# Performance work log

Measured on AMD Instinct MI355X. Metric: run time of the kernel, lower is better.

The kernel has to match this reference:

```python
import math
import jax, jax.numpy as jnp
import numpy as np

S = 2  # scale_factor
IN_CH = 256
OFFSET_FACTOR = math.sqrt(128.0 / IN_CH)


def setup_inputs() -> dict:
    key = jax.random.key(0)
    k1, k2, k3 = jax.random.split(key, 3)
    x = jax.random.normal(k1, (4, IN_CH, 128, 128), jnp.float32)
    conv_w = jax.random.normal(k2, (2 * S * S, IN_CH, 1, 1), jnp.float32) * 0.01
    conv_b = jax.random.normal(k3, (2 * S * S,), jnp.float32) * 0.01
    return {"x": x, "conv_w": conv_w, "conv_b": conv_b}


def reference(x, conv_w, conv_b):
    b, c, H, W = x.shape
    s = S
    # 1x1 conv producing per-subpixel (x, y) offsets: [b, 2*s*s, H, W]
    out = jnp.einsum('bchw,oc->bohw', x, conv_w[:, :, 0, 0]) + conv_b[None, :, None, None]
    o1, o2 = jnp.split(out, 2, axis=1)  # each [b, s*s, H, W]
    # sub-pixel bias grid (meshgrid 'xy'): X[i,j]=x[j], Y[i,j]=y[i]
    sub = jnp.arange(0.0, 1.0, 1.0 / s)
    xb, yb = jnp.meshgrid(sub, sub, indexing='xy')  # [s, s]
    xb = xb.reshape(1, -1, 1, 1)
    yb = yb.reshape(1, -1, 1, 1)
    o1 = OFFSET_FACTOR * o1 + jnp.arange(W)[None, None, None, :] + xb  # x coords (pixels)
    o2 = OFFSET_FACTOR * o2 + jnp.arange(H)[None, None, :, None] + yb  # y coords (pixels)
    # [b,2,s,s,H,W] -> [b,2,H,s,W,s] -> [b,2,N], N = s*H*s*W
    off = jnp.stack((o1, o2), axis=1).reshape(b, 2, s, s, H, W)
    off = off.transpose(0, 1, 4, 2, 5, 3).reshape(b, 2, -1)
    xc, yc = off[:, 0], off[:, 1]  # [b, N]
    x0 = jnp.floor(xc)
    y0 = jnp.floor(yc)
    fx = xc - x0
    fy = yc - y0
    x0i = jnp.clip(x0.astype(jnp.int32), 0, W - 1)
    x1i = jnp.clip(x0.astype(jnp.int32) + 1, 0, W - 1)
    y0i = jnp.clip(y0.astype(jnp.int32), 0, H - 1)
    y1i = jnp.clip(y0.astype(jnp.int32) + 1, 0, H - 1)
    bidx = jnp.arange(b)[:, None]

    def gather(yi, xi):
        return x[bidx, :, yi, xi]  # [b, N, c]

    val = (gather(y0i, x0i) * ((1 - fx) * (1 - fy))[..., None]
           + gather(y0i, x1i) * (fx * (1 - fy))[..., None]
           + gather(y1i, x0i) * ((1 - fx) * fy)[..., None]
           + gather(y1i, x1i) * (fx * fy)[..., None])  # [b, N, c]
    return val.transpose(0, 2, 1).reshape(b, c, s * H, s * W)
```

## Files before the change

### kernel.cpp

```cpp
#include <hip/hip_runtime.h>
#include <math.h>

#define BATCH 4
#define C 256
#define H 128
#define W 128
#define HW (H * W)
#define OH 256
#define OW 256
#define NPIX (BATCH * HW)
#define NPOS (BATCH * OH * OW)
#define KSPLIT 4
#define KCH (C / KSPLIT)
#define CCHUNKS 4
__device__ __constant__ float OFF_FACTOR = 0.70710678118654752f;

__global__ __launch_bounds__(256) void conv_desc_kernel(
    const float* __restrict__ x, const float* __restrict__ cw,
    const float* __restrict__ cb, float2* __restrict__ desc) {
    __shared__ float sw[8 * C];
    __shared__ __align__(16) float red[KSPLIT * 8 * 256];
    int t = threadIdx.x;

    #pragma unroll
    for (int i = 0; i < 8; ++i) sw[i * 256 + t] = cw[i * 256 + t];
    __syncthreads();

    int k = t >> 6;
    int q = t & 63;
    int g4 = blockIdx.x * 64 + q;
    int g = g4 * 4;
    int b = g >> 14;
    int pix = g & (HW - 1);
    const float* xp = x + (size_t)b * C * HW + (size_t)(k * KCH) * HW + pix;

    float4 acc[8];
    #pragma unroll
    for (int o = 0; o < 8; ++o) acc[o] = make_float4(0.f, 0.f, 0.f, 0.f);

    #pragma unroll 8
    for (int c = 0; c < KCH; ++c) {
        float4 v = *(const float4*)(xp + (size_t)c * HW);
        #pragma unroll
        for (int o = 0; o < 8; ++o) {
            float wv = sw[o * C + k * KCH + c];
            acc[o].x += v.x * wv; acc[o].y += v.y * wv;
            acc[o].z += v.z * wv; acc[o].w += v.w * wv;
        }
    }

    #pragma unroll
    for (int o = 0; o < 8; ++o)
        *(float4*)&red[((k * 8 + o) << 8) + (q << 2)] = acc[o];
    __syncthreads();

    int g2 = blockIdx.x * 256 + t;
    int b2 = g2 >> 14;
    int pix2 = g2 & (HW - 1);
    int h2 = pix2 >> 7;
    int w2 = pix2 & (W - 1);

    float s[8];
    #pragma unroll
    for (int o = 0; o < 8; ++o) {
        float a = cb[o];
        #pragma unroll
        for (int kk = 0; kk < KSPLIT; ++kk)
            a += red[((kk * 8 + o) << 8) + t];
        s[o] = a;
    }

    #pragma unroll
    for (int sy = 0; sy < 2; ++sy) {
        int j0 = sy * 2;
        float yb = (float)h2 + 0.5f * (float)sy;
        float xc0 = OFF_FACTOR * s[j0]     + (float)w2;
        float yc0 = OFF_FACTOR * s[4 + j0] + yb;
        float xc1 = OFF_FACTOR * s[j0 + 1] + (float)w2 + 0.5f;
        float yc1 = OFF_FACTOR * s[5 + j0] + yb;
        int p = (b2 * OH + 2 * h2 + sy) * OW + 2 * w2;
        *(float4*)&desc[p] = make_float4(xc0, yc0, xc1, yc1);
    }
}

__global__ __launch_bounds__(256) void sample_kernel(
    const float* __restrict__ x, const float2* __restrict__ desc,
    float* __restrict__ out) {
    int t = threadIdx.x;
    int lin = blockIdx.x;
    int ord = (lin & 7) * 256 + (lin >> 3);
    int cchunk = ord & 3;
    int h = (ord >> 2) & (H - 1);
    int b = ord >> 9;

    int oh0 = 2 * h, oh1 = 2 * h + 1;
    int p0 = (b * OH + oh0) * OW + t;
    int p1 = (b * OH + oh1) * OW + t;
    float2 d0 = desc[p0];
    float2 d1 = desc[p1];

    int4 ia, ib; float4 wa, wb;
    {
        float x0f = floorf(d0.x), y0f = floorf(d0.y);
        float fx = d0.x - x0f, fy = d0.y - y0f;
        int x0 = (int)x0f, y0 = (int)y0f;
        int x0i = min(max(x0, 0), W - 1), x1i = min(max(x0 + 1, 0), W - 1);
        int y0i = min(max(y0, 0), H - 1), y1i = min(max(y0 + 1, 0), H - 1);
        ia = make_int4(y0i * W + x0i, y0i * W + x1i,
                       y1i * W + x0i, y1i * W + x1i);
        wa = make_float4((1.f - fx) * (1.f - fy), fx * (1.f - fy),
                         (1.f - fx) * fy,         fx * fy);
    }
    {
        float x0f = floorf(d1.x), y0f = floorf(d1.y);
        float fx = d1.x - x0f, fy = d1.y - y0f;
        int x0 = (int)x0f, y0 = (int)y0f;
        int x0i = min(max(x0, 0), W - 1), x1i = min(max(x0 + 1, 0), W - 1);
        int y0i = min(max(y0, 0), H - 1), y1i = min(max(y0 + 1, 0), H - 1);
        ib = make_int4(y0i * W + x0i, y0i * W + x1i,
                       y1i * W + x0i, y1i * W + x1i);
        wb = make_float4((1.f - fx) * (1.f - fy), fx * (1.f - fy),
                         (1.f - fx) * fy,         fx * fy);
    }

    int c0 = cchunk * 64;
    const float* xp = x + (size_t)b * C * HW + (size_t)c0 * HW;
    float* op = out + (((size_t)(b * C + c0) * OH + oh0) * OW) + t;

    #pragma unroll 2
    for (int c = 0; c < 64; ++c) {
        const float* pl = xp + (size_t)c * HW;
        float v0 = pl[ia.x] * wa.x + pl[ia.y] * wa.y +
                   pl[ia.z] * wa.z + pl[ia.w] * wa.w;
        float v1 = pl[ib.x] * wb.x + pl[ib.y] * wb.y +
                   pl[ib.z] * wb.z + pl[ib.w] * wb.w;
        float* o0 = op + (size_t)c * (OH * OW);
        __builtin_nontemporal_store(v0, o0);
        __builtin_nontemporal_store(v1, o0 + OW);
    }
}

extern "C" void kernel_launch(void* const* d_in, const int* in_sizes, int n_in,
                              void* d_out, int out_size, void* d_ws, size_t ws_size,
                              hipStream_t stream) {
    const float* x  = (const float*)d_in[0];
    const float* cw = (const float*)d_in[1];
    const float* cb = (const float*)d_in[2];
    float* out = (float*)d_out;

    float2* desc = (float2*)d_ws;

    conv_desc_kernel<<<256, 256, 0, stream>>>(x, cw, cb, desc);
    sample_kernel<<<BATCH * H * CCHUNKS, 256, 0, stream>>>(x, desc, out);
}
```

Measured before the change: 361.6 us.

## Stage input rows in shared memory for bilinear sampling with global fallback

The sample kernel now loads a 4-row by 32-channel input tile into LDS per block. Each thread computes four output sub-pixels, two adjacent pairs on two output rows, from that tile and stores them as float2 pairs. If any lane's offsets fall outside the staged rows, the block falls back to direct global gathers. This swaps scattered global gather loads for LDS reads and wider stores. In exchange it adds a tile-load phase, a barrier and 64KB of LDS per block, which may limit occupancy.

```diff
diff --git a/kernel.cpp b/kernel.cpp
--- a/kernel.cpp
+++ b/kernel.cpp
@@ -8,12 +8,13 @@
 #define HW (H * W)
 #define OH 256
 #define OW 256
-#define NPIX (BATCH * HW)
-#define NPOS (BATCH * OH * OW)
 #define KSPLIT 4
 #define KCH (C / KSPLIT)
-#define CCHUNKS 4
+#define SCH 32
+#define NCHUNK (C / SCH)
 __device__ __constant__ float OFF_FACTOR = 0.70710678118654752f;
+
+typedef float __attribute__((ext_vector_type(2))) f32x2;
 
 __global__ __launch_bounds__(256) void conv_desc_kernel(
     const float* __restrict__ x, const float* __restrict__ cw,
@@ -84,59 +85,98 @@
 }
 
 __global__ __launch_bounds__(256) void sample_kernel(
-    const float* __restrict__ x, const float2* __restrict__ desc,
+    const float* __restrict__ x, const float4* __restrict__ desc4,
     float* __restrict__ out) {
+    __shared__ __align__(16) float tile[SCH * 4 * W];
     int t = threadIdx.x;
     int lin = blockIdx.x;
-    int ord = (lin & 7) * 256 + (lin >> 3);
-    int cchunk = ord & 3;
-    int h = (ord >> 2) & (H - 1);
-    int b = ord >> 9;
+    int xcd = lin & 7;
+    int i8  = lin >> 3;
+    int combo = xcd * 4 + (i8 >> 6);
+    int hblk  = i8 & 63;
+    int b = combo >> 3;
+    int chunk = combo & 7;
+    int h0 = hblk * 2;
+    int c0 = chunk * SCH;
 
-    int oh0 = 2 * h, oh1 = 2 * h + 1;
-    int p0 = (b * OH + oh0) * OW + t;
-    int p1 = (b * OH + oh1) * OW + t;
-    float2 d0 = desc[p0];
-    float2 d1 = desc[p1];
+    const float* xb = x + (size_t)b * C * HW + (size_t)c0 * HW;
 
-    int4 ia, ib; float4 wa, wb;
-    {
-        float x0f = floorf(d0.x), y0f = floorf(d0.y);
-        float fx = d0.x - x0f, fy = d0.y - y0f;
+    #pragma unroll
+    for (int j = 0; j < 16; ++j) {
+        int idx = (j * 256 + t) * 4;
+        int c   = idx >> 9;
+        int i   = (idx >> 7) & 3;
+        int col = idx & 127;
+        int row = min(max(h0 - 1 + i, 0), H - 1);
+        *(float4*)&tile[idx] =
+            *(const float4*)(xb + (size_t)c * HW + row * W + col);
+    }
+
+    int hr = t >> 7;
+    int w  = t & 127;
+    int hh = h0 + hr;
+
+    float4 d0 = desc4[(((size_t)b * OH + 2 * hh) * OW + 2 * w) >> 1];
+    float4 d1 = desc4[(((size_t)b * OH + 2 * hh + 1) * OW + 2 * w) >> 1];
+
+    int   loff[4][4];
+    float wt[4][4];
+    bool allok = true;
+    float xcs[4] = {d0.x, d0.z, d1.x, d1.z};
+    float ycs[4] = {d0.y, d0.w, d1.y, d1.w};
+    #pragma unroll
+    for (int j = 0; j < 4; ++j) {
+        float xc = xcs[j], yc = ycs[j];
+        float x0f = floorf(xc), y0f = floorf(yc);
+        float fx = xc - x0f, fy = yc - y0f;
         int x0 = (int)x0f, y0 = (int)y0f;
         int x0i = min(max(x0, 0), W - 1), x1i = min(max(x0 + 1, 0), W - 1);
         int y0i = min(max(y0, 0), H - 1), y1i = min(max(y0 + 1, 0), H - 1);
-        ia = make_int4(y0i * W + x0i, y0i * W + x1i,
-                       y1i * W + x0i, y1i * W + x1i);
-        wa = make_float4((1.f - fx) * (1.f - fy), fx * (1.f - fy),
-                         (1.f - fx) * fy,         fx * fy);
-    }
-    {
-        float x0f = floorf(d1.x), y0f = floorf(d1.y);
-        float fx = d1.x - x0f, fy = d1.y - y0f;
-        int x0 = (int)x0f, y0 = (int)y0f;
-        int x0i = min(max(x0, 0), W - 1), x1i = min(max(x0 + 1, 0), W - 1);
-        int y0i = min(max(y0, 0), H - 1), y1i = min(max(y0 + 1, 0), H - 1);
-        ib = make_int4(y0i * W + x0i, y0i * W + x1i,
-                       y1i * W + x0i, y1i * W + x1i);
-        wb = make_float4((1.f - fx) * (1.f - fy), fx * (1.f - fy),
-                         (1.f - fx) * fy,         fx * fy);
+        int iy0 = y0i - h0 + 1, iy1 = y1i - h0 + 1;
+        allok = allok && ((unsigned)iy0 <= 3u) && ((unsigned)iy1 <= 3u);
+        loff[j][0] = iy0 * W + x0i;  loff[j][1] = iy0 * W + x1i;
+        loff[j][2] = iy1 * W + x0i;  loff[j][3] = iy1 * W + x1i;
+        wt[j][0] = (1.f - fx) * (1.f - fy); wt[j][1] = fx * (1.f - fy);
+        wt[j][2] = (1.f - fx) * fy;         wt[j][3] = fx * fy;
     }
 
-    int c0 = cchunk * 64;
-    const float* xp = x + (size_t)b * C * HW + (size_t)c0 * HW;
-    float* op = out + (((size_t)(b * C + c0) * OH + oh0) * OW) + t;
+    __syncthreads();
 
-    #pragma unroll 2
-    for (int c = 0; c < 64; ++c) {
-        const float* pl = xp + (size_t)c * HW;
-        float v0 = pl[ia.x] * wa.x + pl[ia.y] * wa.y +
-                   pl[ia.z] * wa.z + pl[ia.w] * wa.w;
-        float v1 = pl[ib.x] * wb.x + pl[ib.y] * wb.y +
-                   pl[ib.z] * wb.z + pl[ib.w] * wb.w;
-        float* o0 = op + (size_t)c * (OH * OW);
-        __builtin_nontemporal_store(v0, o0);
-        __builtin_nontemporal_store(v1, o0 + OW);
+    float* op0 = out + (((size_t)(b * C + c0) * OH + 2 * hh) * OW) + 2 * w;
+
+    if (__all(allok)) {
+        #pragma unroll 4
+        for (int c = 0; c < SCH; ++c) {
+            const float* tl = tile + c * (4 * W);
+            float v[4];
+            #pragma unroll
+            for (int j = 0; j < 4; ++j)
+                v[j] = tl[loff[j][0]] * wt[j][0] + tl[loff[j][1]] * wt[j][1] +
+                       tl[loff[j][2]] * wt[j][2] + tl[loff[j][3]] * wt[j][3];
+            float* op = op0 + (size_t)c * (OH * OW);
+            f32x2 r0 = {v[0], v[1]};
+            f32x2 r1 = {v[2], v[3]};
+            __builtin_nontemporal_store(r0, (f32x2*)op);
+            __builtin_nontemporal_store(r1, (f32x2*)(op + OW));
+        }
+    } else {
+        int rebase = (h0 - 1) * W;
+        #pragma unroll 2
+        for (int c = 0; c < SCH; ++c) {
+            const float* pl = xb + (size_t)c * HW;
+            float v[4];
+            #pragma unroll
+            for (int j = 0; j < 4; ++j)
+                v[j] = pl[loff[j][0] + rebase] * wt[j][0] +
+                       pl[loff[j][1] + rebase] * wt[j][1] +
+                       pl[loff[j][2] + rebase] * wt[j][2] +
+                       pl[loff[j][3] + rebase] * wt[j][3];
+            float* op = op0 + (size_t)c * (OH * OW);
+            f32x2 r0 = {v[0], v[1]};
+            f32x2 r1 = {v[2], v[3]};
+            __builtin_nontemporal_store(r0, (f32x2*)op);
+            __builtin_nontemporal_store(r1, (f32x2*)(op + OW));
+        }
     }
 }
 
@@ -151,5 +191,6 @@
     float2* desc = (float2*)d_ws;
 
     conv_desc_kernel<<<256, 256, 0, stream>>>(x, cw, cb, desc);
-    sample_kernel<<<BATCH * H * CCHUNKS, 256, 0, stream>>>(x, desc, out);
+    sample_kernel<<<BATCH * (H / 2) * NCHUNK, 256, 0, stream>>>(
+        x, (const float4*)desc, out);
 }
```

New measurement: 314.8 us. -12.9%, faster.
